# Kernel tuning notes

Hardware: AMD Instinct MI355X
Metric: run time of the kernel (lower is better)

The kernel has to match this reference:

```python
import jax, jax.numpy as jnp
import numpy as np

TAU = 0.1
B, F_IN, D, K, C = 128, 1000, 512, 10, 5


def setup_inputs() -> dict:
    key = jax.random.key(0)
    ks = jax.random.split(key, 12)
    s = 0.05
    feats = jax.random.normal(ks[0], (B, F_IN), jnp.float32)
    W_adapt = jax.random.normal(ks[1], (F_IN, D), jnp.float32) * s
    b_adapt = jnp.zeros((D,), jnp.float32)
    W_ch = jax.random.normal(ks[2], (C, D, D), jnp.float32) * s   # 5 per-channel Linear(D,D)
    b_ch = jnp.zeros((C, D), jnp.float32)
    W_gate = jax.random.normal(ks[3], (C, D), jnp.float32) * s    # 5 gate Linear(D,1)
    b_gate = jnp.zeros((C,), jnp.float32)
    W_mlp = jax.random.normal(ks[4], (D, K), jnp.float32) * s
    b_mlp = jnp.zeros((K,), jnp.float32)
    T = 1000
    u = jax.random.uniform(ks[5], (B, C, T, 2), jnp.float32, 1e-10, 1.0)
    gumbel = -jnp.log(-jnp.log(u))                                 # Gumbel(0,1) noise, one draw per sample/time
    return {"feats": feats, "W_adapt": W_adapt, "b_adapt": b_adapt,
            "W_ch": W_ch, "b_ch": b_ch, "W_gate": W_gate, "b_gate": b_gate,
            "W_mlp": W_mlp, "b_mlp": b_mlp, "gumbel": gumbel, "repeat_num": T}


def reference(feats, W_adapt, b_adapt, W_ch, b_ch, W_gate, b_gate, W_mlp, b_mlp, gumbel, repeat_num):
    # backbone_output_adapter: Linear(1000, D) + ReLU
    r_b = jax.nn.relu(feats @ W_adapt + b_adapt)                   # [B, D]
    # 5 subjective channels: Linear(D, D) + ReLU each (vectorized over channel axis c)
    h = jax.nn.relu(jnp.einsum('bd,cde->bce', r_b, W_ch) + b_ch)   # [B, C, D]
    # gates: Linear(D, 1) + Sigmoid per channel -> p_t_ [B, C, 1]
    p = jax.nn.sigmoid(jnp.einsum('bcd,cd->bc', h, W_gate) + b_gate)  # [B, C]
    p_t = p[:, :, None]                                            # [B, C, 1]
    # train path: logits = [1-p, p]; repeat_num independent gumbel-softmax draws, vectorized over T
    logits = jnp.stack([1.0 - p, p], axis=-1)                      # [B, C, 2]
    y = jax.nn.softmax((logits[:, :, None, :] + gumbel) / TAU, axis=-1)  # [B, C, T, 2]
    g_t = y[..., 1]                                                # [B, C, T]
    # gate softmax over channel dim, then gated channel mixing
    v_t = jax.nn.softmax(g_t, axis=1)                              # [B, C, T]
    r_g = jnp.einsum('bcd,bct->bdt', h, v_t)                       # [B, D, T]  (256 MB, memory-bound)
    # mlp per time step: Linear(D, K) + ReLU + Softmax(dim=1 over classes)
    logits_s = jax.nn.relu(jnp.einsum('bdt,dk->btk', r_g, W_mlp) + b_mlp)
    r_s = jax.nn.softmax(logits_s, axis=-1)                        # [B, T, K]
    r_s = jnp.transpose(r_s, (1, 0, 2))                            # [T, B, K] == list of T [B,K] outputs
    return (r_s, g_t, p_t)
```

## Files before the change

### kernel.cpp

```cpp
#include <hip/hip_runtime.h>
#include <hip/hip_bf16.h>
#include <math.h>


__global__ __launch_bounds__(256) void kA(const float* __restrict__ feats,
                                          const float* __restrict__ W_adapt,
                                          float* __restrict__ pA) {
    __shared__ float fls[128 * 50];
    __shared__ float wls[50 * 32];
    const int tid = threadIdx.x;
    const int e0 = blockIdx.x * 32;
    const int s  = blockIdx.y;
    const int k0 = s * 50;

    #pragma unroll
    for (int it = 0; it < 25; ++it) {
        int idx = it * 256 + tid;
        int b_l = idx / 50, k_l = idx - b_l * 50;
        fls[idx] = feats[b_l * 1000 + k0 + k_l];
    }
    #pragma unroll
    for (int it = 0; it < 7; ++it) {
        int idx = it * 256 + tid;
        if (idx < 1600)
            wls[idx] = W_adapt[(k0 + (idx >> 5)) * 512 + e0 + (idx & 31)];
    }
    __syncthreads();

    const int ep = tid & 15, bg = tid >> 4;
    float2 acc[8] = {};
    const float* fb = &fls[bg * 8 * 50];
    const float* wb = &wls[ep * 2];
    #pragma unroll 2
    for (int k = 0; k < 50; ++k) {
        float2 w = *(const float2*)&wb[k * 32];
        #pragma unroll
        for (int i = 0; i < 8; ++i) {
            float r = fb[i * 50 + k];
            acc[i].x = fmaf(r, w.x, acc[i].x);
            acc[i].y = fmaf(r, w.y, acc[i].y);
        }
    }
    #pragma unroll
    for (int i = 0; i < 8; ++i)
        *(float2*)&pA[(s * 128 + bg * 8 + i) * 512 + e0 + ep * 2] = acc[i];
}

__global__ __launch_bounds__(256) void kRA(const float* __restrict__ pA,
                                           const float* __restrict__ b_adapt,
                                           float* __restrict__ r_b) {
    int i = blockIdx.x * 256 + threadIdx.x;
    float acc = b_adapt[i & 511];
    #pragma unroll
    for (int s = 0; s < 20; ++s) acc += pA[s * 65536 + i];
    r_b[i] = fmaxf(acc, 0.f);
}

__global__ __launch_bounds__(256) void kB(const float* __restrict__ r_b,
                                          const float* __restrict__ W_ch,
                                          float* __restrict__ pB) {
    __shared__ float rbs[128 * 64];
    __shared__ float wls[64 * 32];
    const int tid = threadIdx.x;
    const int e0 = blockIdx.x * 32;
    const int ds = blockIdx.y;
    const int c  = blockIdx.z;
    const int d0 = ds * 64;

    #pragma unroll
    for (int it = 0; it < 32; ++it) {
        int idx = it * 256 + tid;
        rbs[idx] = r_b[(idx >> 6) * 512 + d0 + (idx & 63)];
    }
    #pragma unroll
    for (int it = 0; it < 8; ++it) {
        int idx = it * 256 + tid;
        wls[idx] = W_ch[((size_t)(c * 512 + d0 + (idx >> 5))) * 512 + e0 + (idx & 31)];
    }
    __syncthreads();

    const int ep = tid & 15, bg = tid >> 4;
    float2 acc[8] = {};
    const float* rb = &rbs[bg * 8 * 64];
    const float* wb = &wls[ep * 2];
    #pragma unroll 2
    for (int d = 0; d < 64; ++d) {
        float2 w = *(const float2*)&wb[d * 32];
        #pragma unroll
        for (int i = 0; i < 8; ++i) {
            float r = rb[i * 64 + d];
            acc[i].x = fmaf(r, w.x, acc[i].x);
            acc[i].y = fmaf(r, w.y, acc[i].y);
        }
    }
    #pragma unroll
    for (int i = 0; i < 8; ++i)
        *(float2*)&pB[((ds * 5 + c) * 128 + bg * 8 + i) * 512 + e0 + ep * 2] = acc[i];
}

__global__ __launch_bounds__(256) void kG(const float* __restrict__ pB,
                                          const float* __restrict__ b_ch,
                                          const float* __restrict__ W_gate,
                                          const float* __restrict__ W_mlp,
                                          const float* __restrict__ b_gate,
                                          float* __restrict__ p,
                                          float* __restrict__ M,
                                          float* __restrict__ out_pt) {
    int wv = threadIdx.x >> 6, lane = threadIdx.x & 63;
    int pair = blockIdx.x * 4 + wv;
    int b = pair / 5, c = pair % 5;
    float gs = 0.f, am[10] = {};
    #pragma unroll
    for (int i = 0; i < 8; ++i) {
        int e = i * 64 + lane;
        float hs = b_ch[c * 512 + e];
        #pragma unroll
        for (int s = 0; s < 8; ++s)
            hs += pB[((s * 5 + c) * 128 + b) * 512 + e];
        float h = fmaxf(hs, 0.f);
        gs = fmaf(h, W_gate[c * 512 + e], gs);
        const float* wm = &W_mlp[e * 10];
        #pragma unroll
        for (int k = 0; k < 10; ++k) am[k] = fmaf(h, wm[k], am[k]);
    }
    #pragma unroll
    for (int off = 32; off; off >>= 1) {
        gs += __shfl_xor(gs, off);
        #pragma unroll
        for (int k = 0; k < 10; ++k) am[k] += __shfl_xor(am[k], off);
    }
    if (lane == 0) {
        float pv = 1.f / (1.f + __expf(-(gs + b_gate[c])));
        p[b * 5 + c] = pv;
        out_pt[b * 5 + c] = pv;
        #pragma unroll
        for (int k = 0; k < 10; ++k) M[(b * 5 + c) * 10 + k] = am[k];
    }
}

__global__ __launch_bounds__(256) void kC(const float* __restrict__ p,
                                          const float* __restrict__ M,
                                          const float* __restrict__ b_mlp,
                                          const float* __restrict__ gumbel,
                                          float* __restrict__ out_rs,
                                          float* __restrict__ out_gt) {
    __shared__ float spv[5];
    __shared__ float sM[50];
    int tid = threadIdx.x;
    int b = blockIdx.y;
    if (tid < 50) sM[tid] = M[b * 50 + tid];
    if (tid < 5)  spv[tid] = p[b * 5 + tid];
    __syncthreads();

    int t = blockIdx.x * 256 + tid;
    if (t >= 1000) return;
    float ex[5], ssum = 0.f;
    #pragma unroll
    for (int c = 0; c < 5; ++c) {
        float2 gu = *(const float2*)&gumbel[(size_t)(((b * 5 + c) * 1000) + t) * 2];
        float arg = (2.f * spv[c] - 1.f + gu.y - gu.x) * 10.0f;
        float gt  = 1.f / (1.f + __expf(-arg));
        out_gt[(b * 5 + c) * 1000 + t] = gt;
        float e = __expf(gt);
        ex[c] = e; ssum += e;
    }
    float inv = 1.f / ssum;
    float lg[10];
    #pragma unroll
    for (int k = 0; k < 10; ++k) lg[k] = b_mlp[k];
    #pragma unroll
    for (int c = 0; c < 5; ++c) {
        float v = ex[c] * inv;
        #pragma unroll
        for (int k = 0; k < 10; ++k) lg[k] = fmaf(v, sM[c * 10 + k], lg[k]);
    }
    float mx = 0.f;
    #pragma unroll
    for (int k = 0; k < 10; ++k) { lg[k] = fmaxf(lg[k], 0.f); mx = fmaxf(mx, lg[k]); }
    float se = 0.f;
    #pragma unroll
    for (int k = 0; k < 10; ++k) { lg[k] = __expf(lg[k] - mx); se += lg[k]; }
    float invs = 1.f / se;
    float2 outv[5];
    #pragma unroll
    for (int k = 0; k < 10; ++k) ((float*)outv)[k] = lg[k] * invs;
    float2* dst = (float2*)&out_rs[(size_t)t * 1280 + b * 10];
    #pragma unroll
    for (int j = 0; j < 5; ++j) dst[j] = outv[j];
}

extern "C" void kernel_launch(void* const* d_in, const int* in_sizes, int n_in,
                              void* d_out, int out_size, void* d_ws, size_t ws_size,
                              hipStream_t stream) {
    const float* feats   = (const float*)d_in[0];
    const float* W_adapt = (const float*)d_in[1];
    const float* b_adapt = (const float*)d_in[2];
    const float* W_ch    = (const float*)d_in[3];
    const float* b_ch    = (const float*)d_in[4];
    const float* W_gate  = (const float*)d_in[5];
    const float* b_gate  = (const float*)d_in[6];
    const float* W_mlp   = (const float*)d_in[7];
    const float* b_mlp   = (const float*)d_in[8];
    const float* gumbel  = (const float*)d_in[9];

    float* out    = (float*)d_out;
    float* out_rs = out;
    float* out_gt = out + 1280000;
    float* out_pt = out + 1920000;

    float* ws  = (float*)d_ws;
    float* pA  = ws;
    float* pB  = pA + 1310720;
    float* r_b = pB + 2621440;
    float* p   = r_b + 65536;
    float* M   = p + 640;

    kA <<<dim3(16, 20),   256, 0, stream>>>(feats, W_adapt, pA);
    kRA<<<256,            256, 0, stream>>>(pA, b_adapt, r_b);
    kB <<<dim3(16, 8, 5), 256, 0, stream>>>(r_b, W_ch, pB);
    kG <<<160,            256, 0, stream>>>(pB, b_ch, W_gate, W_mlp, b_gate, p, M, out_pt);
    kC <<<dim3(4, 128),   256, 0, stream>>>(p, M, b_mlp, gumbel, out_rs, out_gt);
}
```

Baseline: 43.51 us.

## Accumulate channel GEMM via atomics and fuse gate reduction into gumbel-softmax kernel

The channel GEMM kernel now atomically adds its split-K partial sums into a bias-initialised h buffer, which the adapter reduction kernel seeds. This removes the separate partial-sum buffer and its 8-way reduction pass. The gate/MLP projection is folded into the final gumbel/softmax kernel, run per batch row with W_mlp staged in shared memory, which drops one launch and the p/M round trip. The cost is 8-way atomic contention, non-deterministic summation order, and the gate work being recomputed by both time-chunk blocks.

After: 50.43 us. 1.16x slower.

```diff
diff --git a/kernel.cpp b/kernel.cpp
--- a/kernel.cpp
+++ b/kernel.cpp
@@ -48,17 +48,22 @@
 
 __global__ __launch_bounds__(256) void kRA(const float* __restrict__ pA,
                                            const float* __restrict__ b_adapt,
-                                           float* __restrict__ r_b) {
+                                           const float* __restrict__ b_ch,
+                                           float* __restrict__ r_b,
+                                           float* __restrict__ hT) {
     int i = blockIdx.x * 256 + threadIdx.x;
-    float acc = b_adapt[i & 511];
+    int e = i & 511;
+    float acc = b_adapt[e];
     #pragma unroll
     for (int s = 0; s < 20; ++s) acc += pA[s * 65536 + i];
     r_b[i] = fmaxf(acc, 0.f);
-}
-
-__global__ __launch_bounds__(256) void kB(const float* __restrict__ r_b,
-                                          const float* __restrict__ W_ch,
-                                          float* __restrict__ pB) {
+    #pragma unroll
+    for (int c = 0; c < 5; ++c) hT[c * 65536 + i] = b_ch[c * 512 + e];
+}
+
+__global__ __launch_bounds__(256) void kB2(const float* __restrict__ r_b,
+                                           const float* __restrict__ W_ch,
+                                           float* __restrict__ hT) {
     __shared__ float rbs[128 * 64];
     __shared__ float wls[64 * 32];
     const int tid = threadIdx.x;
@@ -94,66 +99,68 @@
         }
     }
     #pragma unroll
-    for (int i = 0; i < 8; ++i)
-        *(float2*)&pB[((ds * 5 + c) * 128 + bg * 8 + i) * 512 + e0 + ep * 2] = acc[i];
-}
-
-__global__ __launch_bounds__(256) void kG(const float* __restrict__ pB,
-                                          const float* __restrict__ b_ch,
-                                          const float* __restrict__ W_gate,
-                                          const float* __restrict__ W_mlp,
-                                          const float* __restrict__ b_gate,
-                                          float* __restrict__ p,
-                                          float* __restrict__ M,
-                                          float* __restrict__ out_pt) {
-    int wv = threadIdx.x >> 6, lane = threadIdx.x & 63;
-    int pair = blockIdx.x * 4 + wv;
-    int b = pair / 5, c = pair % 5;
-    float gs = 0.f, am[10] = {};
-    #pragma unroll
     for (int i = 0; i < 8; ++i) {
-        int e = i * 64 + lane;
-        float hs = b_ch[c * 512 + e];
-        #pragma unroll
-        for (int s = 0; s < 8; ++s)
-            hs += pB[((s * 5 + c) * 128 + b) * 512 + e];
-        float h = fmaxf(hs, 0.f);
-        gs = fmaf(h, W_gate[c * 512 + e], gs);
-        const float* wm = &W_mlp[e * 10];
-        #pragma unroll
-        for (int k = 0; k < 10; ++k) am[k] = fmaf(h, wm[k], am[k]);
-    }
-    #pragma unroll
-    for (int off = 32; off; off >>= 1) {
-        gs += __shfl_xor(gs, off);
-        #pragma unroll
-        for (int k = 0; k < 10; ++k) am[k] += __shfl_xor(am[k], off);
-    }
-    if (lane == 0) {
-        float pv = 1.f / (1.f + __expf(-(gs + b_gate[c])));
-        p[b * 5 + c] = pv;
-        out_pt[b * 5 + c] = pv;
-        #pragma unroll
-        for (int k = 0; k < 10; ++k) M[(b * 5 + c) * 10 + k] = am[k];
-    }
-}
-
-__global__ __launch_bounds__(256) void kC(const float* __restrict__ p,
-                                          const float* __restrict__ M,
-                                          const float* __restrict__ b_mlp,
-                                          const float* __restrict__ gumbel,
-                                          float* __restrict__ out_rs,
-                                          float* __restrict__ out_gt) {
-    __shared__ float spv[5];
-    __shared__ float sM[50];
-    int tid = threadIdx.x;
-    int b = blockIdx.y;
-    if (tid < 50) sM[tid] = M[b * 50 + tid];
-    if (tid < 5)  spv[tid] = p[b * 5 + tid];
-    __syncthreads();
-
-    int t = blockIdx.x * 256 + tid;
-    if (t >= 1000) return;
+        float* dst = &hT[(c * 128 + bg * 8 + i) * 512 + e0 + ep * 2];
+        atomicAdd(dst,     acc[i].x);
+        atomicAdd(dst + 1, acc[i].y);
+    }
+}
+
+__global__ __launch_bounds__(512) void kCG(const float* __restrict__ hT,
+                                           const float* __restrict__ W_gate,
+                                           const float* __restrict__ W_mlp,
+                                           const float* __restrict__ b_gate,
+                                           const float* __restrict__ b_mlp,
+                                           const float* __restrict__ gumbel,
+                                           float* __restrict__ out_rs,
+                                           float* __restrict__ out_gt,
+                                           float* __restrict__ out_pt) {
+    __shared__ float sWm[5120];
+    __shared__ float red[5][11];
+    __shared__ float spv[5], sM[50];
+    const int tid = threadIdx.x;
+    const int tc = blockIdx.x, b = blockIdx.y;
+
+    #pragma unroll
+    for (int it = 0; it < 10; ++it) sWm[it * 512 + tid] = W_mlp[it * 512 + tid];
+    __syncthreads();
+
+    const int wv = tid >> 6, lane = tid & 63;
+    if (wv < 5) {
+        const int c = wv;
+        float gs = 0.f, am[10] = {};
+        #pragma unroll
+        for (int i = 0; i < 8; ++i) {
+            int e = i * 64 + lane;
+            float h = fmaxf(hT[(c * 128 + b) * 512 + e], 0.f);
+            gs = fmaf(h, W_gate[c * 512 + e], gs);
+            const float* wm = &sWm[e * 10];
+            #pragma unroll
+            for (int k = 0; k < 10; ++k) am[k] = fmaf(h, wm[k], am[k]);
+        }
+        #pragma unroll
+        for (int off = 32; off; off >>= 1) {
+            gs += __shfl_xor(gs, off);
+            #pragma unroll
+            for (int k = 0; k < 10; ++k) am[k] += __shfl_xor(am[k], off);
+        }
+        if (lane == 0) {
+            red[c][0] = gs;
+            #pragma unroll
+            for (int k = 0; k < 10; ++k) red[c][1 + k] = am[k];
+        }
+    }
+    __syncthreads();
+    if (tid < 5) {
+        float pv = 1.f / (1.f + __expf(-(red[tid][0] + b_gate[tid])));
+        spv[tid] = pv;
+        if (tc == 0) out_pt[b * 5 + tid] = pv;
+    }
+    if (tid < 50) sM[tid] = red[tid / 10][1 + tid % 10];
+    __syncthreads();
+
+    int t = tc * 500 + tid;
+    if (tid >= 500) return;
     float ex[5], ssum = 0.f;
     #pragma unroll
     for (int c = 0; c < 5; ++c) {
@@ -210,14 +217,12 @@
 
     float* ws  = (float*)d_ws;
     float* pA  = ws;
-    float* pB  = pA + 1310720;
-    float* r_b = pB + 2621440;
-    float* p   = r_b + 65536;
-    float* M   = p + 640;
+    float* r_b = pA + 1310720;
+    float* hT  = r_b + 65536;
 
     kA <<<dim3(16, 20),   256, 0, stream>>>(feats, W_adapt, pA);
-    kRA<<<256,            256, 0, stream>>>(pA, b_adapt, r_b);
-    kB <<<dim3(16, 8, 5), 256, 0, stream>>>(r_b, W_ch, pB);
-    kG <<<160,            256, 0, stream>>>(pB, b_ch, W_gate, W_mlp, b_gate, p, M, out_pt);
-    kC <<<dim3(4, 128),   256, 0, stream>>>(p, M, b_mlp, gumbel, out_rs, out_gt);
-}
+    kRA<<<256,            256, 0, stream>>>(pA, b_adapt, b_ch, r_b, hT);
+    kB2<<<dim3(16, 8, 5), 256, 0, stream>>>(r_b, W_ch, hT);
+    kCG<<<dim3(2, 128),   512, 0, stream>>>(hT, W_gate, W_mlp, b_gate, b_mlp,
+                                            gumbel, out_rs, out_gt, out_pt);
+}
```
